# Performance work log

Hardware: AMD Instinct MI355X
Metric: run time of the kernel (lower is better)

## Reference

```python
import jax, jax.numpy as jnp
import numpy as np

K_SIM_SCHEDULE = [4, 8, 16]
K_CON_SCHEDULE = [2, 4, 8]
NEG = 1000000000.0


def _dual_adjacency(h, k_sim, k_con):
    """Binary causal dual adjacency (similar / dissimilar), no gradient."""
    B, T, D = h.shape
    h = jax.lax.stop_gradient(h)
    xn = h / jnp.maximum(jnp.linalg.norm(h, axis=-1, keepdims=True), 1e-12)
    sim = jnp.einsum('btd,bsd->bts', xn, xn)                 # (B,T,T)
    past = jnp.tril(jnp.ones((T, T), h.dtype), -1)           # strictly-past mask
    sim = sim * past - NEG * (1.0 - past)
    eff_sim = min(k_sim, T - 1)
    eff_con = min(k_con, max(0, T - 1 - eff_sim))
    bI = jnp.arange(B)[:, None, None]
    tI = jnp.arange(T)[None, :, None]
    A_sim = jnp.zeros((B, T, T), h.dtype)
    if eff_sim > 0:
        _, top_idx = jax.lax.top_k(sim, eff_sim)             # (B,T,k)
        A_sim = A_sim.at[bI, tI, top_idx].set(1.0) * past
    A_con = jnp.zeros((B, T, T), h.dtype)
    if eff_con > 0:
        sim_con = jnp.where(A_sim > 0, NEG, sim)
        _, bot_idx = jax.lax.top_k(-sim_con, eff_con)        # smallest eff_con
        A_con = A_con.at[bI, tI, bot_idx].set(1.0) * past * (1.0 - A_sim)
    return A_sim, A_con


def _aggregate(h, A):
    # unweighted mean over selected neighbors; empty rows -> zeros
    deg = jnp.sum(A, axis=-1, keepdims=True)
    return jnp.einsum('bts,bsd->btd', A, h) / jnp.maximum(deg, 1.0)


def setup_inputs() -> dict:
    key = jax.random.key(0)
    ks = jax.random.split(key, 2)
    B, T, D, R = 4, 2048, 512, 3
    x = jax.random.normal(ks[0], (B, T, D), dtype=jnp.float32)
    gain = jnp.ones((R, D), dtype=jnp.float32)
    bias = jnp.zeros((R, D), dtype=jnp.float32)
    log_mix = jnp.zeros((R,), dtype=jnp.float32)
    log_alpha = jnp.zeros((R,), dtype=jnp.float32)
    log_momentum = jnp.asarray(1.0, dtype=jnp.float32)
    log_scale = jnp.asarray(0.0, dtype=jnp.float32)
    return {"x": x, "gain": gain, "bias": bias, "log_mix": log_mix,
            "log_alpha": log_alpha, "log_momentum": log_momentum,
            "log_scale": log_scale}


def reference(x, gain, bias, log_mix, log_alpha, log_momentum, log_scale):
    momentum = jax.nn.sigmoid(log_momentum)
    scale = jax.nn.softplus(log_scale) + 0.01
    h = x
    for r in range(len(K_SIM_SCHEDULE)):
        mix = jax.nn.sigmoid(log_mix[r])
        alpha = jax.nn.sigmoid(log_alpha[r])
        A_sim, A_con = _dual_adjacency(h, K_SIM_SCHEDULE[r], K_CON_SCHEDULE[r])
        msg_pos = _aggregate(h, A_sim)
        msg_neg = _aggregate(h, A_con)
        ctx = alpha * msg_pos + (1.0 - alpha) * msg_neg
        blended = mix * h + (1.0 - mix) * ctx
        h_new = jax.nn.gelu(blended * gain[r] + bias[r], approximate=False)
        h = momentum * h + (1.0 - momentum) * h_new
    return (h - x) * scale
```

## Files before the change

### kernel.cpp

```cpp
#include <hip/hip_runtime.h>
#include <hip/hip_bf16.h>
#include <cstdint>
#include <cstddef>

#define BB 4
#define TT 2048
#define DD 512
#define NEG_INF (-3.402823466e+38f)
#define POS_INF (3.402823466e+38f)

typedef __attribute__((ext_vector_type(8))) short bf16x8;
typedef __attribute__((ext_vector_type(8))) unsigned short ushort8;
typedef __attribute__((ext_vector_type(4))) float f32x4;

__device__ __forceinline__ float sigmoidf_(float x){ return 1.0f/(1.0f+expf(-x)); }

__device__ __forceinline__ unsigned short f2bf(float x){
  __hip_bfloat16 b = __float2bfloat16(x);
  return *reinterpret_cast<unsigned short*>(&b);
}

__device__ __forceinline__ unsigned int fwd_map(float f){
  unsigned int b = __float_as_uint(f);
  return b ^ ((b & 0x80000000u) ? 0xFFFFFFFFu : 0x80000000u);
}
__device__ __forceinline__ float inv_map(unsigned int u){
  unsigned int b = (u & 0x80000000u) ? (u ^ 0x80000000u) : ~u;
  return __uint_as_float(b);
}

__device__ __forceinline__ unsigned long long shfl_xor64(unsigned long long x, int off){
  unsigned int hi = __shfl_xor((unsigned int)(x >> 32), off);
  unsigned int lo = __shfl_xor((unsigned int)x, off);
  return ((unsigned long long)hi << 32) | lo;
}

__global__ __launch_bounds__(64) void k_normsplit(const float* __restrict__ h, float* __restrict__ rnorm,
                                                  unsigned short* __restrict__ Xh, unsigned short* __restrict__ Xl){
  int row = blockIdx.x;
  const float* hr = h + (size_t)row*DD;
  int lane = threadIdx.x;
  float4 v0 = *(const float4*)&hr[lane*4];
  float4 v1 = *(const float4*)&hr[lane*4 + 256];
  float ss = v0.x*v0.x+v0.y*v0.y+v0.z*v0.z+v0.w*v0.w
           + v1.x*v1.x+v1.y*v1.y+v1.z*v1.z+v1.w*v1.w;
  #pragma unroll
  for (int off=32; off; off>>=1) ss += __shfl_xor(ss, off);
  float rn = 1.0f / fmaxf(sqrtf(ss), 1e-12f);
  if (lane==0) rnorm[row] = rn;

  float xs[8] = {v0.x,v0.y,v0.z,v0.w,v1.x,v1.y,v1.z,v1.w};
  unsigned short hb[8], lb[8];
  #pragma unroll
  for (int q=0;q<8;q++){
    float xn = xs[q]*rn;
    unsigned short hh = f2bf(xn);
    __hip_bfloat16 bh = *reinterpret_cast<__hip_bfloat16*>(&hh);
    float rem = xn - __bfloat162float(bh);
    hb[q] = hh; lb[q] = f2bf(rem);
  }
  ushort4 h0 = {hb[0],hb[1],hb[2],hb[3]}, h1 = {hb[4],hb[5],hb[6],hb[7]};
  ushort4 l0 = {lb[0],lb[1],lb[2],lb[3]}, l1 = {lb[4],lb[5],lb[6],lb[7]};
  *(ushort4*)&Xh[(size_t)row*DD + lane*4]       = h0;
  *(ushort4*)&Xh[(size_t)row*DD + lane*4 + 256] = h1;
  *(ushort4*)&Xl[(size_t)row*DD + lane*4]       = l0;
  *(ushort4*)&Xl[(size_t)row*DD + lane*4 + 256] = l1;
}

__global__ __launch_bounds__(256) void k_sim(const unsigned short* __restrict__ Xh,
                                             const unsigned short* __restrict__ Xl,
                                             float* __restrict__ sim,
                                             unsigned short* __restrict__ keys, int b0){
  int p = blockIdx.x;
  int jt = (int)((sqrtf(8.0f*(float)p + 1.0f) - 1.0f)*0.5f);
  while ((jt+1)*(jt+2)/2 <= p) jt++;
  while (jt*(jt+1)/2 > p) jt--;
  int is = p - jt*(jt+1)/2;

  int bl = blockIdx.y;
  size_t xoff = (size_t)(b0 + bl)*TT*DD;
  const unsigned short* XhB = Xh + xoff;
  const unsigned short* XlB = Xl + xoff;
  float* simb = sim + (size_t)bl*TT*TT;
  unsigned short* keyb = keys + (size_t)bl*TT*TT;
  int t0 = jt*128, s0 = is*128;

  __shared__ __align__(16) short As[128*32];
  __shared__ __align__(16) short Bs[128*32];

  int tid = threadIdx.x, wave = tid>>6, lane = tid&63;
  int wr = wave>>1, wc = wave&1;

  int srow = tid>>2;
  int sc8  = (tid&3)*8;

  f32x4 acc[4][4];
  #pragma unroll
  for (int m=0;m<4;m++)
    #pragma unroll
    for (int n=0;n<4;n++) acc[m][n] = (f32x4){0.f,0.f,0.f,0.f};

  ushort8 ra0, ra1, rb0, rb1;
  auto gload = [&](int s){
    int pass = s>>4; int kcol = (s&15)*32;
    const unsigned short* sA = (pass<2) ? XhB : XlB;
    const unsigned short* sB = (pass!=1) ? XhB : XlB;
    ra0 = *(const ushort8*)&sA[(size_t)(t0+srow)*DD + kcol + sc8];
    ra1 = *(const ushort8*)&sA[(size_t)(t0+srow+64)*DD + kcol + sc8];
    rb0 = *(const ushort8*)&sB[(size_t)(s0+srow)*DD + kcol + sc8];
    rb1 = *(const ushort8*)&sB[(size_t)(s0+srow+64)*DD + kcol + sc8];
  };

  gload(0);
  for (int s=0; s<48; ++s){
    __syncthreads();
    *(ushort8*)&As[srow*32 + sc8]      = ra0;
    *(ushort8*)&As[(srow+64)*32 + sc8] = ra1;
    *(ushort8*)&Bs[srow*32 + sc8]      = rb0;
    *(ushort8*)&Bs[(srow+64)*32 + sc8] = rb1;
    __syncthreads();
    if (s < 47) gload(s+1);

    int arow = wr*64 + (lane&15);
    int brow = wc*64 + (lane&15);
    int kb = (lane>>4)*8;
    bf16x8 af[4], bf[4];
    #pragma unroll
    for (int m=0;m<4;m++) af[m] = *(const bf16x8*)&As[(arow + m*16)*32 + kb];
    #pragma unroll
    for (int n=0;n<4;n++) bf[n] = *(const bf16x8*)&Bs[(brow + n*16)*32 + kb];
    #pragma unroll
    for (int m=0;m<4;m++)
      #pragma unroll
      for (int n=0;n<4;n++)
        acc[m][n] = __builtin_amdgcn_mfma_f32_16x16x32_bf16(af[m], bf[n], acc[m][n], 0, 0, 0);
  }

  #pragma unroll
  for (int m=0;m<4;m++){
    int t = t0 + wr*64 + m*16 + (lane>>4)*4;
    #pragma unroll
    for (int n=0;n<4;n++){
      int sc = s0 + wc*64 + n*16 + (lane&15);
      float* dst = simb + (size_t)t*TT + sc;
      unsigned short* kdst = keyb + (size_t)t*TT + sc;
      #pragma unroll
      for (int j=0;j<4;j++){
        float v = acc[m][n][j];
        dst[(size_t)j*TT] = v;
        kdst[(size_t)j*TT] = (unsigned short)(fwd_map(v) >> 16);
      }
    }
  }
}

#define BMASK 0xFFFFFF00u

#define KLO(D,S) ( ((D) << 16)         | (0x7FFu - (unsigned int)(S)) )
#define KHI(D,S) ( ((D) & 0xFFFF0000u) | (0x7FFu - (unsigned int)(S)) )
#define INS32(KK) do{ unsigned int a=(KK); \
  if (a > kv3){ unsigned int d0=kv3; if (d0 > cert) cert = d0; \
    if (a > kv0){ unsigned int q=kv0; kv0=a; a=q; } \
    if (a > kv1){ unsigned int q=kv1; kv1=a; a=q; } \
    if (a > kv2){ unsigned int q=kv2; kv2=a; a=q; } \
    kv3=a; } \
  else { if (a > cert) cert = a; } }while(0)
#define PROC8(W,S) { INS32(KLO((W).x,(S)));   INS32(KHI((W).x,(S)+1)); \
                     INS32(KLO((W).y,(S)+2)); INS32(KHI((W).y,(S)+3)); \
                     INS32(KLO((W).z,(S)+4)); INS32(KHI((W).z,(S)+5)); \
                     INS32(KLO((W).w,(S)+6)); INS32(KHI((W).w,(S)+7)); }

__device__ __forceinline__ unsigned int radix24(const float* __restrict__ srow, int t, int k1,
                                                unsigned int flip, int* sh, int lane){
  #pragma unroll
  for (int i=0;i<4;i++) sh[lane + i*64] = 0;
  int t4 = t & ~3;
  for (int s4 = lane*4; s4 < t4; s4 += 256){
    float4 f = *(const float4*)&srow[s4];
    unsigned int u0=fwd_map(f.x)^flip, u1=fwd_map(f.y)^flip, u2=fwd_map(f.z)^flip, u3=fwd_map(f.w)^flip;
    atomicAdd(&sh[u0>>24],1); atomicAdd(&sh[u1>>24],1);
    atomicAdd(&sh[u2>>24],1); atomicAdd(&sh[u3>>24],1);
  }
  for (int s = t4 + lane; s < t; s += 64){
    unsigned int u = fwd_map(srow[s])^flip;
    atomicAdd(&sh[u>>24],1);
  }
  unsigned int pfx = 0u; int kp = k1;
  #pragma unroll
  for (int pass = 0; pass < 3; ++pass){
    int shift = 24 - 8*pass;
    int m4 = sh[4*lane] + sh[4*lane+1] + sh[4*lane+2] + sh[4*lane+3];
    int x = __shfl(m4, 63-lane);
    #pragma unroll
    for (int off = 1; off < 64; off <<= 1){
      int v = __shfl_up(x, off);
      if (lane >= off) x += v;
    }
    int T = __shfl(x, 63-lane);
    int G = T - m4;
    bool hit = (G < kp) && (kp <= T);
    unsigned int npfx = 0u; int nkp = 0;
    if (hit){
      int c = G; int D = 4*lane;
      #pragma unroll
      for (int i = 3; i >= 0; --i){
        int hc = sh[4*lane + i];
        if (kp <= c + hc){ D = 4*lane + i; break; }
        c += hc;
      }
      npfx = pfx | ((unsigned int)D << shift);
      nkp = kp - c;
    }
    unsigned long long hm = __ballot(hit);
    int src = __ffsll(hm) - 1;
    pfx = __shfl(npfx, src);
    kp  = __shfl(nkp, src);
    if (pass == 2) break;

    int nshift = shift - 8;
    unsigned int keep = 0xFFFFFFFFu << shift;
    #pragma unroll
    for (int i=0;i<4;i++) sh[lane + i*64] = 0;
    for (int s4 = lane*4; s4 < t4; s4 += 256){
      float4 f = *(const float4*)&srow[s4];
      unsigned int u0=fwd_map(f.x)^flip, u1=fwd_map(f.y)^flip, u2=fwd_map(f.z)^flip, u3=fwd_map(f.w)^flip;
      if (((u0 ^ pfx) & keep) == 0) atomicAdd(&sh[(u0>>nshift)&255],1);
      if (((u1 ^ pfx) & keep) == 0) atomicAdd(&sh[(u1>>nshift)&255],1);
      if (((u2 ^ pfx) & keep) == 0) atomicAdd(&sh[(u2>>nshift)&255],1);
      if (((u3 ^ pfx) & keep) == 0) atomicAdd(&sh[(u3>>nshift)&255],1);
    }
    for (int s = t4 + lane; s < t; s += 64){
      unsigned int u = fwd_map(srow[s])^flip;
      if (((u ^ pfx) & keep) == 0) atomicAdd(&sh[(u>>nshift)&255],1);
    }
  }
  return pfx;
}

template<int ESIM, int ECON>
__global__ __launch_bounds__(256) void k_topk(const float* __restrict__ sim,
                                              const unsigned short* __restrict__ keys, int b0,
                                              const float* __restrict__ h, const float* __restrict__ rnorm,
                                              int* __restrict__ topidx, int* __restrict__ botidx,
                                              int* __restrict__ bcnt){
  constexpr int K1  = ESIM + 8;
  constexpr int K1B = ESIM + ECON + 8;
  constexpr int CANDCAP = 40;
  constexpr int EQCAP = 44;
  constexpr float TAU = 5e-5f;
  __shared__ int s_hist[4][256];
  __shared__ int s_cand[4][CANDCAP];
  __shared__ int s_eq[4][EQCAP];
  __shared__ int s_sel[4][ESIM];
  __shared__ int s_bot[4][16];
  __shared__ int s_cnt[4][2];

  int tid = threadIdx.x, lane = tid & 63, wid = tid >> 6;
  int lrow = blockIdx.x*4 + wid;
  int bl = lrow >> 11, t = lrow & (TT-1);
  int gb = b0 + bl;
  int grow = (gb << 11) | t;

  if (t <= ESIM){
    if (lane < t) topidx[(size_t)grow*16 + lane] = lane;
    if (lane == 0) bcnt[grow] = 0;
    return;
  }
  const float* srow = sim + (size_t)lrow*TT;
  const unsigned short* krow = keys + (size_t)lrow*TT;
  const float* hb  = h + (size_t)gb*TT*DD;
  const float* rnb = rnorm + (size_t)gb*TT;

  int* sh    = s_hist[wid];
  int* scand = s_cand[wid];
  int* seq   = s_eq[wid];
  int* ssel  = s_sel[wid];
  int* sbot  = s_bot[wid];
  int t4 = t & ~3;

  unsigned int kv0=0, kv1=0, kv2=0, kv3=0, cert=0;
  {
    int nd  = t >> 1;
    int nd4 = nd >> 2;
    const uint4* kr4 = (const uint4*)krow;
    uint4 w0, w1, w2, w3;
    bool g0 = (lane       < nd4);
    bool g1 = (lane +  64 < nd4);
    bool g2 = (lane + 128 < nd4);
    bool g3 = (lane + 192 < nd4);
    if (g0) w0 = kr4[lane];
    if (g1) w1 = kr4[lane + 64];
    if (g2) w2 = kr4[lane + 128];
    if (g3) w3 = kr4[lane + 192];
    if (g0) PROC8(w0, (lane)*8);
    if (g1) PROC8(w1, (lane+64)*8);
    if (g2) PROC8(w2, (lane+128)*8);
    if (g3) PROC8(w3, (lane+192)*8);
    for (int d = nd4*4 + lane; d < nd; d += 64){
      unsigned int w = ((const unsigned int*)krow)[d];
      int s = 2*d;
      INS32(KLO(w, s)); INS32(KHI(w, s+1));
    }
    if ((t & 1) && lane == 0){
      unsigned int u16 = krow[t-1];
      INS32((u16 << 16) | (0x7FFu - (unsigned int)(t-1)));
    }
  }

  int ck = (kv0?1:0) + (kv1?1:0) + (kv2?1:0) + (kv3?1:0);
  {
  }
  unsigned long long kb0=__ballot(ck&1), kb1=__ballot(ck&2), kb2=__ballot(ck&4);
  int kept = __popcll(kb0) + 2*__popcll(kb1) + 4*__popcll(kb2);
  int ncand = min(min(t, K1), kept);

  bool fb;
  if (ncand > ESIM){
    unsigned int v = 0;
    for (int bit = 31; bit >= 0; --bit){
      unsigned int test = v | (1u << bit);
      int c = (kv0>=test) + (kv1>=test) + (kv2>=test) + (kv3>=test);
      unsigned long long c0=__ballot(c&1), c1=__ballot(c&2), c2=__ballot(c&4);
      int cnt = __popcll(c0) + 2*__popcll(c1) + 4*__popcll(c2);
      if (cnt >= ncand) v = test;
    }
    unsigned int m = 0;
    if (kv0 < v) m = kv0;
    else if (kv1 < v) m = kv1;
    else if (kv2 < v) m = kv2;
    else if (kv3 < v) m = kv3;
    unsigned int mo = (cert > m) ? cert : m;
    #pragma unroll
    for (int off=32; off; off>>=1){
      unsigned int om = __shfl_xor(mo, off);
      if (om > mo) mo = om;
    }
    unsigned int b_out = mo >> 16;

    int ci = (kv0>=v) + (kv1>=v) + (kv2>=v) + (kv3>=v);
    unsigned long long p0=__ballot(ci&1), p1=__ballot(ci&2), p2=__ballot(ci&4);
    unsigned long long below = (lane == 0) ? 0ull : ((~0ull) >> (64 - lane));
    int pre = __popcll(p0&below) + 2*__popcll(p1&below) + 4*__popcll(p2&below);
    if (ci > 0) scand[pre]   = 0x7FF - (int)(kv0 & 0x7FFu);
    if (ci > 1) scand[pre+1] = 0x7FF - (int)(kv1 & 0x7FFu);
    if (ci > 2) scand[pre+2] = 0x7FF - (int)(kv2 & 0x7FFu);
    if (ci > 3) scand[pre+3] = 0x7FF - (int)(kv3 & 0x7FFu);

    unsigned long long key = 0ull;
    if (lane < ncand){
      int idx = scand[lane];
      float f = srow[idx];
      key = (((unsigned long long)fwd_map(f)) << 32) | (unsigned int)(~idx);
    }

    unsigned long long nk = ~key;
    #pragma unroll
    for (int kk = 2; kk <= 32; kk <<= 1){
      #pragma unroll
      for (int j = kk >> 1; j > 0; j >>= 1){
        unsigned long long o = shfl_xor64(nk, j);
        bool keepMin = (((lane & kk) == 0) == ((lane & j) == 0));
        bool less = (nk < o);
        nk = (keepMin == less) ? nk : o;
      }
    }
    key = ~nk;

    int   sidx = (int)(~(unsigned int)key);
    float val  = inv_map((unsigned int)(key >> 32));
    float vA = __shfl(val, ESIM-1);
    float vB = __shfl(val, ESIM);
    unsigned int b17 = __shfl((unsigned int)(key >> 48), ESIM);

    fb = (b_out >= b17) || (vA - vB < TAU);
    if (!fb && lane < ESIM){
      ssel[lane] = sidx;
      topidx[(size_t)grow*16 + lane] = sidx;
    }
  } else {
    fb = true;
  }

  if (fb){
    int k1 = min(t, K1);
    unsigned int thr = radix24(srow, t, k1, 0u, sh, lane);

    if (lane == 0){ s_cnt[wid][0] = 0; s_cnt[wid][1] = 0; }
    for (int s4 = lane*4; s4 < t4; s4 += 256){
      float4 f = *(const float4*)&srow[s4];
      unsigned int uu[4] = {fwd_map(f.x), fwd_map(f.y), fwd_map(f.z), fwd_map(f.w)};
      #pragma unroll
      for (int q=0;q<4;q++){
        unsigned int b24 = uu[q] & BMASK;
        if (b24 > thr){ int p = atomicAdd(&s_cnt[wid][0],1); if (p < CANDCAP) scand[p] = s4+q; }
        else if (b24 == thr){ int p = atomicAdd(&s_cnt[wid][1],1); if (p < EQCAP) seq[p] = s4+q; }
      }
    }
    for (int s = t4 + lane; s < t; s += 64){
      unsigned int b24 = fwd_map(srow[s]) & BMASK;
      if (b24 > thr){ int p = atomicAdd(&s_cnt[wid][0],1); if (p < CANDCAP) scand[p] = s; }
      else if (b24 == thr){ int p = atomicAdd(&s_cnt[wid][1],1); if (p < EQCAP) seq[p] = s; }
    }
    int c_gt = min(s_cnt[wid][0], CANDCAP);
    int c_eq = min(s_cnt[wid][1], EQCAP);
    int ncand2 = min(c_gt + c_eq, 64);

    unsigned int myu = 0u; int myi = 0x7fffffff;
    if (lane < ncand2){
      myi = (lane < c_gt) ? scand[lane] : seq[lane - c_gt];
      myu = fwd_map(srow[myi]);
    }

    float fvA = 0.f, fvB = 0.f;
    {
      unsigned int cu = myu; int ci2 = myi;
      #pragma unroll
      for (int k = 0; k <= ESIM; ++k){
        unsigned int bu = cu; int bi = ci2;
        #pragma unroll
        for (int off=32; off; off>>=1){
          unsigned int ou = __shfl_xor(bu, off); int oi = __shfl_xor(bi, off);
          if (ou > bu || (ou == bu && oi < bi)){ bu = ou; bi = oi; }
        }
        if (k < ESIM && lane == 0) ssel[k] = bi;
        if (k == ESIM-1) fvA = inv_map(bu);
        if (k == ESIM)   fvB = inv_map(bu);
        if (ci2 == bi){ cu = 0u; ci2 = 0x7fffffff; }
      }
    }

    bool resc = (fvA - fvB < TAU);
    if (resc){
      const float* hq = hb + (size_t)t*DD;
      float rt = rnb[t];
      float4 qq0 = *(const float4*)&hq[lane*4];
      float4 qq1 = *(const float4*)&hq[lane*4 + 256];
      float ev = NEG_INF;
      for (int j = 0; j < ncand2; ++j){
        int idx = (j < c_gt) ? scand[j] : seq[j - c_gt];
        const float* hc = hb + (size_t)idx*DD;
        float4 c0 = *(const float4*)&hc[lane*4];
        float4 c1 = *(const float4*)&hc[lane*4 + 256];
        float pp = qq0.x*c0.x+qq0.y*c0.y+qq0.z*c0.z+qq0.w*c0.w
                 + qq1.x*c1.x+qq1.y*c1.y+qq1.z*c1.z+qq1.w*c1.w;
        #pragma unroll
        for (int off=32; off; off>>=1) pp += __shfl_xor(pp, off);
        float ex = pp * rt * rnb[idx];
        if (lane == j) ev = ex;
      }
      float rv = (lane < ncand2) ? ev : NEG_INF;
      int   ri = myi;
      #pragma unroll
      for (int k = 0; k < ESIM; ++k){
        float bv = rv; int bi = ri;
        #pragma unroll
        for (int off=32; off; off>>=1){
          float ov = __shfl_xor(bv, off); int oi = __shfl_xor(bi, off);
          if (ov > bv || (ov == bv && oi < bi)){ bv = ov; bi = oi; }
        }
        if (lane == 0) ssel[k] = bi;
        if (ri == bi) rv = NEG_INF;
      }
    }
    if (lane < ESIM) topidx[(size_t)grow*16 + lane] = ssel[lane];
  }

  int need = ECON - (TT - t);
  int cnt2 = 0;
  if (need > 0){
    constexpr unsigned int FLIP = 0xFFFFFFFFu;
    int k1b = min(t, K1B);
    unsigned int thrb = radix24(srow, t, k1b, FLIP, sh, lane);

    if (lane == 0){ s_cnt[wid][0] = 0; s_cnt[wid][1] = 0; }
    for (int s4 = lane*4; s4 < t4; s4 += 256){
      float4 f = *(const float4*)&srow[s4];
      unsigned int uu[4] = {fwd_map(f.x)^FLIP, fwd_map(f.y)^FLIP, fwd_map(f.z)^FLIP, fwd_map(f.w)^FLIP};
      #pragma unroll
      for (int q=0;q<4;q++){
        unsigned int b24 = uu[q] & BMASK;
        if (b24 > thrb){ int p = atomicAdd(&s_cnt[wid][0],1); if (p < CANDCAP) scand[p] = s4+q; }
        else if (b24 == thrb){ int p = atomicAdd(&s_cnt[wid][1],1); if (p < EQCAP) seq[p] = s4+q; }
      }
    }
    for (int s = t4 + lane; s < t; s += 64){
      unsigned int u = fwd_map(srow[s])^FLIP;
      unsigned int b24 = u & BMASK;
      if (b24 > thrb){ int p = atomicAdd(&s_cnt[wid][0],1); if (p < CANDCAP) scand[p] = s; }
      else if (b24 == thrb){ int p = atomicAdd(&s_cnt[wid][1],1); if (p < EQCAP) seq[p] = s; }
    }
    int bc_gt = min(s_cnt[wid][0], CANDCAP);
    int bc_eq = min(s_cnt[wid][1], EQCAP);
    int ncb = min(bc_gt + bc_eq, 64);

    unsigned int mu = 0u; int mi = 0x7fffffff;
    if (lane < ncb){
      mi = (lane < bc_gt) ? scand[lane] : seq[lane - bc_gt];
      mu = fwd_map(srow[mi]) ^ FLIP;
    }
    float wA = 0.f, wB = 0.f;
    unsigned int cu = mu; int ci3 = mi;
    #pragma unroll
    for (int k = 0; k < K1B; ++k){
      if (k < ncb && cnt2 < need + 8){
        unsigned int bu = cu; int bi = ci3;
        #pragma unroll
        for (int off=32; off; off>>=1){
          unsigned int ou = __shfl_xor(bu, off); int oi = __shfl_xor(bi, off);
          if (ou > bu || (ou == bu && oi < bi)){ bu = ou; bi = oi; }
        }
        if (ci3 == bi){ cu = 0u; ci3 = 0x7fffffff; }
        bool mem = false;
        #pragma unroll
        for (int j=0;j<ESIM;j++) if (ssel[j] == bi) mem = true;
        if (!mem){
          if (lane == 0) sbot[cnt2] = bi;
          float val = inv_map(bu ^ FLIP);
          if (cnt2 == need-1) wA = val;
          if (cnt2 == need)   wB = val;
          cnt2++;
        }
      }
    }
    int npick = min(need, cnt2);
    bool rb = (cnt2 > need) && (wB - wA < TAU);
    if (!rb){
      if (lane < npick) botidx[(size_t)grow*8 + lane] = sbot[lane];
    } else {
      const float* hq = hb + (size_t)t*DD;
      float rt = rnb[t];
      float4 qq0 = *(const float4*)&hq[lane*4];
      float4 qq1 = *(const float4*)&hq[lane*4 + 256];
      float ev = POS_INF; int ei = 0x7fffffff;
      for (int j = 0; j < cnt2; ++j){
        int idx = sbot[j];
        const float* hc = hb + (size_t)idx*DD;
        float4 c0 = *(const float4*)&hc[lane*4];
        float4 c1 = *(const float4*)&hc[lane*4 + 256];
        float pp = qq0.x*c0.x+qq0.y*c0.y+qq0.z*c0.z+qq0.w*c0.w
                 + qq1.x*c1.x+qq1.y*c1.y+qq1.z*c1.z+qq1.w*c1.w;
        #pragma unroll
        for (int off=32; off; off>>=1) pp += __shfl_xor(pp, off);
        float ex = pp * rt * rnb[idx];
        if (lane == j){ ev = ex; ei = idx; }
      }
      #pragma unroll
      for (int k = 0; k < ECON; ++k){
        if (k < npick){
          float bv = ev; int bi = ei;
          #pragma unroll
          for (int off=32; off; off>>=1){
            float ov = __shfl_xor(bv, off); int oi = __shfl_xor(bi, off);
            if (ov < bv || (ov == bv && oi < bi)){ bv = ov; bi = oi; }
          }
          if (lane == 0) botidx[(size_t)grow*8 + k] = bi;
          if (ei == bi) ev = POS_INF;
        }
      }
    }
    cnt2 = npick;
  }
  if (lane == 0) bcnt[grow] = cnt2;
}

__global__ __launch_bounds__(256) void k_agg(const float* __restrict__ hsrc, float* __restrict__ hdst,
                                             const int* __restrict__ topidx, const int* __restrict__ botidx,
                                             const int* __restrict__ bcnt,
                                             const float* __restrict__ gain, const float* __restrict__ bias,
                                             const float* __restrict__ log_mix, const float* __restrict__ log_alpha,
                                             const float* __restrict__ log_momentum, int r, int eff_sim){
  int row = blockIdx.x;
  int b = row >> 11; int t = row & (TT-1);
  int n_sim = min(eff_sim, t);
  int n_con = bcnt[row];
  float mix      = sigmoidf_(log_mix[r]);
  float alpha    = sigmoidf_(log_alpha[r]);
  float momentum = sigmoidf_(log_momentum[0]);
  const float* hb = hsrc + (size_t)b*TT*DD;

  __shared__ int sidx[16];
  __shared__ int scidx[8];
  if (threadIdx.x < 16) sidx[threadIdx.x]  = (threadIdx.x < n_sim) ? topidx[(size_t)row*16 + threadIdx.x] : 0;
  if (threadIdx.x < 8)  scidx[threadIdx.x] = (threadIdx.x < n_con) ? botidx[(size_t)row*8  + threadIdx.x] : 0;
  __syncthreads();

  #pragma unroll
  for (int e = threadIdx.x; e < DD; e += 256){
    float sp = 0.f;
    for (int j=0;j<n_sim;j++) sp += hb[(size_t)sidx[j]*DD + e];
    float sn = 0.f;
    for (int j=0;j<n_con;j++) sn += hb[(size_t)scidx[j]*DD + e];
    float mp = sp / (float)max(n_sim, 1);
    float mn = sn / (float)max(n_con, 1);
    float ctx = alpha*mp + (1.f-alpha)*mn;
    float hv = hsrc[(size_t)row*DD + e];
    float blended = mix*hv + (1.f-mix)*ctx;
    float u = blended*gain[e] + bias[e];
    float g = 0.5f*u*(1.0f + erff(u*0.7071067811865475f));
    hdst[(size_t)row*DD + e] = momentum*hv + (1.f-momentum)*g;
  }
}

__global__ __launch_bounds__(256) void k_final(const float* __restrict__ hfin, const float* __restrict__ x,
                                               const float* __restrict__ log_scale, float* __restrict__ out, int n){
  float scale = log1pf(expf(log_scale[0])) + 0.01f;
  int i = blockIdx.x*256 + threadIdx.x;
  if (i < n) out[i] = (hfin[i] - x[i]) * scale;
}

extern "C" void kernel_launch(void* const* d_in, const int* in_sizes, int n_in,
                              void* d_out, int out_size, void* d_ws, size_t ws_size,
                              hipStream_t stream) {
  const float* x         = (const float*)d_in[0];
  const float* gain      = (const float*)d_in[1];
  const float* bias      = (const float*)d_in[2];
  const float* log_mix   = (const float*)d_in[3];
  const float* log_alpha = (const float*)d_in[4];
  const float* log_mom   = (const float*)d_in[5];
  const float* log_scale = (const float*)d_in[6];

  float* hA = (float*)d_out;
  char* ws = (char*)d_ws;
  size_t off = 0;
  auto alloc = [&](size_t bytes){ void* p = ws + off; off += (bytes + 255) & ~(size_t)255; return p; };

  float*          hB     = (float*)alloc((size_t)BB*TT*DD*4);
  float*          rnorm  = (float*)alloc((size_t)BB*TT*4);
  int*            topidx = (int*)  alloc((size_t)BB*TT*16*4);
  int*            botidx = (int*)  alloc((size_t)BB*TT*8*4);
  int*            bcnt   = (int*)  alloc((size_t)BB*TT*4);
  unsigned short* Xh     = (unsigned short*)alloc((size_t)BB*TT*DD*2);
  unsigned short* Xl     = (unsigned short*)alloc((size_t)BB*TT*DD*2);

  size_t rem = (ws_size > off) ? (ws_size - off) : 0;
  int cb = (int)(rem / ((size_t)TT*TT*6 + 512));
  if (cb < 1) cb = 1;
  if (cb > BB) cb = BB;
  float*          sim  = (float*)alloc((size_t)cb*TT*TT*4);
  unsigned short* keys = (unsigned short*)alloc((size_t)cb*TT*TT*2);

  const float* hsrc = x;
  float* hdst = hB;
  const int ks[3] = {4, 8, 16};

  for (int r = 0; r < 3; ++r){
    k_normsplit<<<BB*TT, 64, 0, stream>>>(hsrc, rnorm, Xh, Xl);
    for (int b0 = 0; b0 < BB; b0 += cb){
      int nb = (BB - b0 < cb) ? (BB - b0) : cb;
      dim3 g(136, nb);
      k_sim<<<g, 256, 0, stream>>>(Xh, Xl, sim, keys, b0);
      if (r == 0)      k_topk<4,2><<<nb*TT/4, 256, 0, stream>>>(sim, keys, b0, hsrc, rnorm, topidx, botidx, bcnt);
      else if (r == 1) k_topk<8,4><<<nb*TT/4, 256, 0, stream>>>(sim, keys, b0, hsrc, rnorm, topidx, botidx, bcnt);
      else             k_topk<16,8><<<nb*TT/4, 256, 0, stream>>>(sim, keys, b0, hsrc, rnorm, topidx, botidx, bcnt);
    }
    k_agg<<<BB*TT, 256, 0, stream>>>(hsrc, hdst, topidx, botidx, bcnt,
                                     gain + (size_t)r*DD, bias + (size_t)r*DD,
                                     log_mix, log_alpha, log_mom, r, ks[r]);
    if (r == 0){ hsrc = hB; hdst = hA; }
    else if (r == 1){ hsrc = hA; hdst = hB; }
  }
  k_final<<<(BB*TT*DD)/256, 256, 0, stream>>>(hB, x, log_scale, (float*)d_out, BB*TT*DD);
}
```

Baseline: 464.5 us.

## Sort packed 16-bit keys and add bf16-threshold rescan before radix fallback

The candidate sort now runs on packed 32-bit keys (bf16 prefix plus index) instead of reloading fp32 values and sorting 64-bit keys. Selection is accepted directly when the bf16 bucket gap alone certifies the top-k separation. Otherwise a second-chance path rescans the 16-bit key row, collects candidates at or above the boundary bucket, and sorts them exactly with a 64-lane bitonic network. The full radix fallback then runs only when that rescan overflows or ties within tolerance. This adds branches and an extra pass over the key row in exchange for avoiding the costly radix select more often.

After: 482.1 us (median of 2 runs). 1.04x slower.

```diff
diff --git a/kernel.cpp b/kernel.cpp
--- a/kernel.cpp
+++ b/kernel.cpp
@@ -159,10 +159,10 @@
 #define KLO(D,S) ( ((D) << 16)         | (0x7FFu - (unsigned int)(S)) )
 #define KHI(D,S) ( ((D) & 0xFFFF0000u) | (0x7FFu - (unsigned int)(S)) )
 #define INS32(KK) do{ unsigned int a=(KK); \
-  if (a > kv3){ unsigned int d0=kv3; if (d0 > cert) cert = d0; \
-    if (a > kv0){ unsigned int q=kv0; kv0=a; a=q; } \
-    if (a > kv1){ unsigned int q=kv1; kv1=a; a=q; } \
-    if (a > kv2){ unsigned int q=kv2; kv2=a; a=q; } \
+  if (a > kv3){ unsigned int q=kv3; if (q > cert) cert = q; \
+    if (a > kv0){ q=kv0; kv0=a; a=q; } \
+    if (a > kv1){ q=kv1; kv1=a; a=q; } \
+    if (a > kv2){ q=kv2; kv2=a; a=q; } \
     kv3=a; } \
   else { if (a > cert) cert = a; } }while(0)
 #define PROC8(W,S) { INS32(KLO((W).x,(S)));   INS32(KHI((W).x,(S)+1)); \
@@ -245,7 +245,7 @@
                                               int* __restrict__ bcnt){
   constexpr int K1  = ESIM + 8;
   constexpr int K1B = ESIM + ECON + 8;
-  constexpr int CANDCAP = 40;
+  constexpr int CANDCAP = 44;
   constexpr int EQCAP = 44;
   constexpr float TAU = 5e-5f;
   __shared__ int s_hist[4][256];
@@ -277,6 +277,7 @@
   int* ssel  = s_sel[wid];
   int* sbot  = s_bot[wid];
   int t4 = t & ~3;
+  unsigned long long below = (lane == 0) ? 0ull : ((~0ull) >> (64 - lane));
 
   unsigned int kv0=0, kv1=0, kv2=0, kv3=0, cert=0;
   {
@@ -308,13 +309,11 @@
   }
 
   int ck = (kv0?1:0) + (kv1?1:0) + (kv2?1:0) + (kv3?1:0);
-  {
-  }
   unsigned long long kb0=__ballot(ck&1), kb1=__ballot(ck&2), kb2=__ballot(ck&4);
   int kept = __popcll(kb0) + 2*__popcll(kb1) + 4*__popcll(kb2);
   int ncand = min(min(t, K1), kept);
 
-  bool fb;
+  bool fb = false, done = false;
   if (ncand > ESIM){
     unsigned int v = 0;
     for (int bit = 31; bit >= 0; --bit){
@@ -335,47 +334,110 @@
       unsigned int om = __shfl_xor(mo, off);
       if (om > mo) mo = om;
     }
-    unsigned int b_out = mo >> 16;
+    unsigned int b_out16 = mo >> 16;
 
     int ci = (kv0>=v) + (kv1>=v) + (kv2>=v) + (kv3>=v);
     unsigned long long p0=__ballot(ci&1), p1=__ballot(ci&2), p2=__ballot(ci&4);
-    unsigned long long below = (lane == 0) ? 0ull : ((~0ull) >> (64 - lane));
     int pre = __popcll(p0&below) + 2*__popcll(p1&below) + 4*__popcll(p2&below);
-    if (ci > 0) scand[pre]   = 0x7FF - (int)(kv0 & 0x7FFu);
-    if (ci > 1) scand[pre+1] = 0x7FF - (int)(kv1 & 0x7FFu);
-    if (ci > 2) scand[pre+2] = 0x7FF - (int)(kv2 & 0x7FFu);
-    if (ci > 3) scand[pre+3] = 0x7FF - (int)(kv3 & 0x7FFu);
-
-    unsigned long long key = 0ull;
-    if (lane < ncand){
-      int idx = scand[lane];
-      float f = srow[idx];
-      key = (((unsigned long long)fwd_map(f)) << 32) | (unsigned int)(~idx);
-    }
-
-    unsigned long long nk = ~key;
+    if (ci > 0) scand[pre]   = (int)kv0;
+    if (ci > 1) scand[pre+1] = (int)kv1;
+    if (ci > 2) scand[pre+2] = (int)kv2;
+    if (ci > 3) scand[pre+3] = (int)kv3;
+
+    unsigned int pk = (lane < ncand) ? (unsigned int)scand[lane] : 0u;
+    unsigned int npk = ~pk;
     #pragma unroll
     for (int kk = 2; kk <= 32; kk <<= 1){
       #pragma unroll
       for (int j = kk >> 1; j > 0; j >>= 1){
-        unsigned long long o = shfl_xor64(nk, j);
+        unsigned int o = __shfl_xor(npk, j);
         bool keepMin = (((lane & kk) == 0) == ((lane & j) == 0));
-        bool less = (nk < o);
-        nk = (keepMin == less) ? nk : o;
-      }
-    }
-    key = ~nk;
-
-    int   sidx = (int)(~(unsigned int)key);
-    float val  = inv_map((unsigned int)(key >> 32));
-    float vA = __shfl(val, ESIM-1);
-    float vB = __shfl(val, ESIM);
-    unsigned int b17 = __shfl((unsigned int)(key >> 48), ESIM);
-
-    fb = (b_out >= b17) || (vA - vB < TAU);
-    if (!fb && lane < ESIM){
-      ssel[lane] = sidx;
-      topidx[(size_t)grow*16 + lane] = sidx;
+        bool less = (npk < o);
+        npk = (keepMin == less) ? npk : o;
+      }
+    }
+    pk = ~npk;
+
+    unsigned int pA = __shfl(pk, ESIM-1);
+    unsigned int pB = __shfl(pk, ESIM);
+    unsigned int bA = pA >> 16, bB = pB >> 16;
+    unsigned int M  = (bB > b_out16) ? bB : b_out16;
+
+    bool t1 = false;
+    if (bA > M && M < 0xFFFFu){
+      float loA = inv_map(bA << 16);
+      float hiM = inv_map((M + 1) << 16);
+      t1 = (loA - hiM >= TAU);
+    }
+    if (t1){
+      if (lane < ESIM){
+        int idx = 0x7FF - (int)(pk & 0xFFFFu);
+        ssel[lane] = idx;
+        topidx[(size_t)grow*16 + lane] = idx;
+      }
+      done = true;
+    } else {
+      unsigned int thc = bB;
+      int cnt = 0;
+      int nd = t >> 1;
+      const unsigned int* kd = (const unsigned int*)krow;
+      for (int d0 = 0; d0 < nd; d0 += 64){
+        int d = d0 + lane;
+        bool in = (d < nd);
+        unsigned int w = in ? kd[d] : 0u;
+        bool e0 = in && ((w & 0xFFFFu) >= thc);
+        bool e1 = in && ((w >> 16)     >= thc);
+        unsigned long long m0 = __ballot(e0), m1 = __ballot(e1);
+        int n0 = __popcll(m0);
+        int bpos0 = cnt + __popcll(m0 & below);
+        int bpos1 = cnt + n0 + __popcll(m1 & below);
+        if (e0 && bpos0 < CANDCAP) scand[bpos0] = 2*d;
+        if (e1 && bpos1 < CANDCAP) scand[bpos1] = 2*d + 1;
+        cnt += n0 + __popcll(m1);
+      }
+      if (t & 1){
+        unsigned int kk16 = krow[t-1];
+        if (kk16 >= thc){
+          if (lane == 0 && cnt < CANDCAP) scand[cnt] = t-1;
+          cnt++;
+        }
+      }
+      if (cnt > CANDCAP){
+        fb = true;
+      } else {
+        int nc = cnt;
+        unsigned long long key = 0ull;
+        if (lane < nc){
+          int idx = scand[lane];
+          float f = srow[idx];
+          key = (((unsigned long long)fwd_map(f)) << 32) | (unsigned int)(~idx);
+        }
+        unsigned long long nk = ~key;
+        #pragma unroll
+        for (int kk = 2; kk <= 64; kk <<= 1){
+          #pragma unroll
+          for (int j = kk >> 1; j > 0; j >>= 1){
+            unsigned long long o = shfl_xor64(nk, j);
+            bool keepMin = (((lane & kk) == 0) == ((lane & j) == 0));
+            bool less = (nk < o);
+            nk = (keepMin == less) ? nk : o;
+          }
+        }
+        key = ~nk;
+        int   idx_l = (int)(~(unsigned int)key);
+        float val   = inv_map((unsigned int)(key >> 32));
+        float vA = __shfl(val, ESIM-1);
+        float vB = __shfl(val, ESIM);
+        if (vA - vB < TAU){
+          fb = true;
+        } else {
+          if (lane < ESIM){
+            ssel[lane] = idx_l;
+            topidx[(size_t)grow*16 + lane] = idx_l;
+          }
+          done = true;
+        }
+      }
     }
   } else {
     fb = true;
```
